# Performance work log

Measured on AMD Instinct MI355X. Metric: run time of the kernel, lower is better.

Reference implementation:

```python
import jax, jax.numpy as jnp
import numpy as np

NUM_EMBEDDINGS = 8192
EMBEDDING_DIM = 512
COMMITMENT_COST = 0.1


def setup_inputs() -> dict:
    key = jax.random.key(0)
    k_z, k_cb = jax.random.split(key)
    z = jax.random.normal(k_z, (16, 1024, EMBEDDING_DIM), dtype=jnp.float32)
    # nn.Embedding weight init: uniform(-1/num_embeddings, 1/num_embeddings)
    bound = 1.0 / NUM_EMBEDDINGS
    codebook = jax.random.uniform(
        k_cb, (NUM_EMBEDDINGS, EMBEDDING_DIM), dtype=jnp.float32,
        minval=-bound, maxval=bound)
    return {"z": z, "codebook": codebook}


def reference(z, codebook):
    # z: [B, T, D], codebook: [K, D]
    zf = z.reshape(-1, z.shape[-1])                      # [N, D]
    # squared euclidean distances: ||z||^2 + ||e||^2 - 2 z e^T  -> [N, K]
    distances = (jnp.sum(zf * zf, axis=1, keepdims=True)
                 + jnp.sum(codebook * codebook, axis=1)
                 - 2.0 * jnp.matmul(zf, codebook.T))
    indices = jnp.argmin(distances, axis=1)              # [N]
    z_quantized = codebook[indices].reshape(z.shape)     # [B, T, D]
    zq_sg = jax.lax.stop_gradient(z_quantized)
    commitment_loss = jnp.mean((zq_sg - z) ** 2)
    # mse(z, zq.detach()) == mse(zq.detach(), z) == commitment_loss
    vq_loss = commitment_loss + COMMITMENT_COST * commitment_loss
    # straight-through estimator
    z_st = z + jax.lax.stop_gradient(z_quantized - z)
    return (z_st, vq_loss)
```

## Files before the change

kernel.cpp:

```cpp
#include <hip/hip_runtime.h>


#define M_ROWS 16384
#define K_CODES 8192
#define DIM 512
#define BM 128
#define BN 128
#define BK 128
#define NT (K_CODES / BN)
#define OUT0_SIZE (M_ROWS * DIM)
#define GB_BLOCKS 1024

typedef int   i32x8 __attribute__((ext_vector_type(8)));
typedef float f32x4 __attribute__((ext_vector_type(4)));

template <bool HI>
__device__ __forceinline__ int pk8(float a, float b, int old) {
    return __builtin_amdgcn_cvt_pk_fp8_f32(a, b, old, HI);
}

__device__ __forceinline__ void gload_lds(const unsigned char* g, unsigned char* l) {
    __builtin_amdgcn_global_load_lds((const __attribute__((address_space(1))) void*)g,
                                     (__attribute__((address_space(3))) void*)l, 16, 0, 0);
}

__global__ __launch_bounds__(256) void convert_all(
    const float* __restrict__ z, const float* __restrict__ cb,
    unsigned char* __restrict__ z8, unsigned char* __restrict__ cb8,
    float* __restrict__ enorm, unsigned int* __restrict__ candMin,
    float* __restrict__ lossSlot)
{
    const int tid = threadIdx.x;
    if (blockIdx.x == 0 && tid == 0) *lossSlot = 0.f;
    {
        int gi = blockIdx.x * 256 + tid;
        if (gi < M_ROWS) candMin[gi] = 0xFFFFFFFFu;
    }
    if (blockIdx.x < K_CODES / 4) {
        const int w = tid >> 6, lane = tid & 63;
        const int row = blockIdx.x * 4 + w;
        const float* src = cb + (size_t)row * DIM + lane * 8;
        float4 a = *(const float4*)(src);
        float4 b = *(const float4*)(src + 4);
        float ns = a.x * a.x + a.y * a.y + a.z * a.z + a.w * a.w
                 + b.x * b.x + b.y * b.y + b.z * b.z + b.w * b.w;
        const float S = 8192.0f;
        int lo = 0, hi = 0;
        lo = pk8<false>(a.x * S, a.y * S, lo); lo = pk8<true>(a.z * S, a.w * S, lo);
        hi = pk8<false>(b.x * S, b.y * S, hi); hi = pk8<true>(b.z * S, b.w * S, hi);
        *(int2*)(cb8 + (size_t)row * DIM + lane * 8) = make_int2(lo, hi);
        for (int m = 32; m; m >>= 1) ns += __shfl_down(ns, m, 64);
        if (lane == 0) enorm[row] = S * ns;
    } else {
        size_t i = ((size_t)(blockIdx.x - K_CODES / 4) * 256 + tid) * 8;
        float4 a = *(const float4*)(z + i);
        float4 b = *(const float4*)(z + i + 4);
        int lo = 0, hi = 0;
        lo = pk8<false>(a.x, a.y, lo); lo = pk8<true>(a.z, a.w, lo);
        hi = pk8<false>(b.x, b.y, hi); hi = pk8<true>(b.z, b.w, hi);
        *(int2*)(z8 + i) = make_int2(lo, hi);
    }
}

__global__ __launch_bounds__(256, 2) void gemm_argmin(
    const unsigned char* __restrict__ z8, const unsigned char* __restrict__ cbb,
    const float* __restrict__ enorm, unsigned int* __restrict__ candMin)
{
    __shared__ alignas(32) unsigned char As[2 * BM * BK];
    __shared__ alignas(32) unsigned char Bs[2 * BN * BK];
    __shared__ float Es[BN];

    const int tid = threadIdx.x;
    const int lane = tid & 63;
    const int w = tid >> 6;
    const int b = blockIdx.x;
    const int xcd = b & 7;
    const int idx = b >> 3;
    const int ktile = idx >> 4;
    const int mtile = xcd * 16 + (idx & 15);
    const int mbase = mtile * BM;
    const int nbase = ktile * BN;

    if (tid < BN) Es[tid] = enorm[nbase + tid];

    f32x4 acc[16];
#pragma unroll
    for (int i = 0; i < 16; ++i) acc[i] = (f32x4){0.f, 0.f, 0.f, 0.f};

    const int rA = lane >> 3;
    const int jG = ((lane & 7) ^ rA) * 16;
    const int quad = lane >> 4;
    const int l15 = lane & 15;
    const int sw = l15 & 7;
    const int rw = (w >> 1) * 64;
    const int cw = (w & 1) * 64;
    const int t32 = ((quad << 1) ^ (sw & 6)) * 16;

#define STAGE(buf, dt_) do {                                                  \
    _Pragma("unroll")                                                         \
    for (int i_ = 0; i_ < 4; ++i_) {                                          \
        int c_ = w * 4 + i_;                                                  \
        int row_ = c_ * 8 + rA;                                               \
        int col_ = (dt_) * BK + jG;                                           \
        gload_lds(z8 + (size_t)(mbase + row_) * DIM + col_,                   \
                  As + (buf) * (BM * BK) + c_ * 1024 + lane * 16);            \
        gload_lds(cbb + (size_t)(nbase + row_) * DIM + col_,                  \
                  Bs + (buf) * (BN * BK) + c_ * 1024 + lane * 16);            \
    } } while (0)

    STAGE(0, 0);
    __syncthreads();

#pragma unroll 1
    for (int dt = 0; dt < 4; ++dt) {
        const int cur = dt & 1;
        if (dt < 3) STAGE(cur ^ 1, dt + 1);
        const unsigned char* Ab = As + cur * (BM * BK);
        const unsigned char* Bb = Bs + cur * (BN * BK);
#pragma unroll
        for (int h = 0; h < 2; ++h) {
            i32x8 bf0 = *(const i32x8*)(Bb + (cw + (h * 2 + 0) * 16 + l15) * BK + t32);
            i32x8 bf1 = *(const i32x8*)(Bb + (cw + (h * 2 + 1) * 16 + l15) * BK + t32);
#pragma unroll
            for (int rf = 0; rf < 4; ++rf) {
                i32x8 a = *(const i32x8*)(Ab + (rw + rf * 16 + l15) * BK + t32);
                acc[rf * 4 + h * 2 + 0] = __builtin_amdgcn_mfma_scale_f32_16x16x128_f8f6f4(
                    a, bf0, acc[rf * 4 + h * 2 + 0],
                    0, 0, 0, 0x7F7F7F7F, 0, 0x7F7F7F7F);
                acc[rf * 4 + h * 2 + 1] = __builtin_amdgcn_mfma_scale_f32_16x16x128_f8f6f4(
                    a, bf1, acc[rf * 4 + h * 2 + 1],
                    0, 0, 0, 0x7F7F7F7F, 0, 0x7F7F7F7F);
            }
        }
        __syncthreads();
    }
#undef STAGE

    float es[4];
#pragma unroll
    for (int cf = 0; cf < 4; ++cf) es[cf] = Es[cw + cf * 16 + l15];

#pragma unroll
    for (int rf = 0; rf < 4; ++rf) {
#pragma unroll
        for (int r = 0; r < 4; ++r) {
            float bv = 3.4e38f; int bi = 0;
#pragma unroll
            for (int cf = 0; cf < 4; ++cf) {
                int col = cw + cf * 16 + l15;
                float dist = fmaf(-2.0f, acc[rf * 4 + cf][r], es[cf]);
                if (dist < bv) { bv = dist; bi = col; }
            }
            unsigned u = __builtin_bit_cast(unsigned, bv);
            u ^= ((unsigned)(((int)u) >> 31)) | 0x80000000u;
            unsigned key = (u & 0xFFFFE000u) | (unsigned)(nbase + bi);
#pragma unroll
            for (int m = 1; m < 16; m <<= 1) {
                unsigned o = __shfl_xor(key, m, 64);
                key = o < key ? o : key;
            }
            if (l15 == 0)
                atomicMin(&candMin[mbase + rw + rf * 16 + quad * 4 + r], key);
        }
    }
}

__global__ __launch_bounds__(256) void gather_out(
    const float* __restrict__ z, const float* __restrict__ cb,
    const unsigned int* __restrict__ candMin, float* __restrict__ out)
{
    __shared__ float red[4];
    const int tid = threadIdx.x;
    const int w = tid >> 6, lane = tid & 63;
    float lsum = 0.f;
#pragma unroll
    for (int it = 0; it < M_ROWS / (GB_BLOCKS * 4); ++it) {
        int row = (it * GB_BLOCKS + blockIdx.x) * 4 + w;
        int k = (int)(candMin[row] & 8191u);
#pragma unroll
        for (int j = 0; j < 2; ++j) {
            int slot = lane + j * 64;
            float4 zv = ((const float4*)(z + (size_t)row * DIM))[slot];
            float4 cv = ((const float4*)(cb + (size_t)k * DIM))[slot];
            float dx = cv.x - zv.x, dy = cv.y - zv.y;
            float dz2 = cv.z - zv.z, dw = cv.w - zv.w;
            float4 o = {zv.x + dx, zv.y + dy, zv.z + dz2, zv.w + dw};
            ((float4*)(out + (size_t)row * DIM))[slot] = o;
            lsum += dx * dx + dy * dy + dz2 * dz2 + dw * dw;
        }
    }
    for (int m = 32; m; m >>= 1) lsum += __shfl_down(lsum, m, 64);
    if (lane == 0) red[w] = lsum;
    __syncthreads();
    if (tid == 0) {
        float t = (red[0] + red[1]) + (red[2] + red[3]);
        atomicAdd(out + OUT0_SIZE, t * (1.1f / (float)OUT0_SIZE));
    }
}

extern "C" void kernel_launch(void* const* d_in, const int* in_sizes, int n_in,
                              void* d_out, int out_size, void* d_ws, size_t ws_size,
                              hipStream_t stream) {
    const float* z = (const float*)d_in[0];
    const float* cb = (const float*)d_in[1];
    float* out = (float*)d_out;
    char* ws = (char*)d_ws;

    unsigned char* z8     = (unsigned char*)(ws);
    unsigned char* cb8    = (unsigned char*)(ws + 8388608);
    float* enorm          = (float*)(ws + 12582912);
    unsigned int* candMin = (unsigned int*)(ws + 12615680);

    convert_all<<<K_CODES / 4 + M_ROWS * DIM / 2048, 256, 0, stream>>>(
        z, cb, z8, cb8, enorm, candMin, out + OUT0_SIZE);
    gemm_argmin<<<NT * (M_ROWS / BM), 256, 0, stream>>>(z8, cb8, enorm, candMin);
    gather_out<<<GB_BLOCKS, 256, 0, stream>>>(z, cb, candMin, out);
}
```

Measured before the change: 249.3 us.

## Single-buffer GEMM LDS tiles to raise occupancy to four blocks per CU

Replaces the double-buffered LDS staging in the fp8 GEMM/argmin kernel with a single buffer (32KB instead of 64KB) and raises the launch-bounds minimum blocks per CU from 2 to 4. The aim is to hide global-load latency through more resident blocks rather than software prefetch. In exchange, each block now waits on its own loads every K-step and adds a barrier per iteration. Tighter register limits could also cause spills with the 16 accumulator vectors.

```diff
diff --git a/kernel.cpp b/kernel.cpp
--- a/kernel.cpp
+++ b/kernel.cpp
@@ -62,12 +62,12 @@
     }
 }
 
-__global__ __launch_bounds__(256, 2) void gemm_argmin(
+__global__ __launch_bounds__(256, 4) void gemm_argmin(
     const unsigned char* __restrict__ z8, const unsigned char* __restrict__ cbb,
     const float* __restrict__ enorm, unsigned int* __restrict__ candMin)
 {
-    __shared__ alignas(32) unsigned char As[2 * BM * BK];
-    __shared__ alignas(32) unsigned char Bs[2 * BN * BK];
+    __shared__ alignas(32) unsigned char As[BM * BK];
+    __shared__ alignas(32) unsigned char Bs[BN * BK];
     __shared__ float Es[BN];
 
     const int tid = threadIdx.x;
@@ -96,34 +96,26 @@
     const int cw = (w & 1) * 64;
     const int t32 = ((quad << 1) ^ (sw & 6)) * 16;
 
-#define STAGE(buf, dt_) do {                                                  \
-    _Pragma("unroll")                                                         \
-    for (int i_ = 0; i_ < 4; ++i_) {                                          \
-        int c_ = w * 4 + i_;                                                  \
-        int row_ = c_ * 8 + rA;                                               \
-        int col_ = (dt_) * BK + jG;                                           \
-        gload_lds(z8 + (size_t)(mbase + row_) * DIM + col_,                   \
-                  As + (buf) * (BM * BK) + c_ * 1024 + lane * 16);            \
-        gload_lds(cbb + (size_t)(nbase + row_) * DIM + col_,                  \
-                  Bs + (buf) * (BN * BK) + c_ * 1024 + lane * 16);            \
-    } } while (0)
-
-    STAGE(0, 0);
-    __syncthreads();
-
 #pragma unroll 1
     for (int dt = 0; dt < 4; ++dt) {
-        const int cur = dt & 1;
-        if (dt < 3) STAGE(cur ^ 1, dt + 1);
-        const unsigned char* Ab = As + cur * (BM * BK);
-        const unsigned char* Bb = Bs + cur * (BN * BK);
+#pragma unroll
+        for (int i_ = 0; i_ < 4; ++i_) {
+            int c_ = w * 4 + i_;
+            int row_ = c_ * 8 + rA;
+            int col_ = dt * BK + jG;
+            gload_lds(z8 + (size_t)(mbase + row_) * DIM + col_,
+                      As + c_ * 1024 + lane * 16);
+            gload_lds(cbb + (size_t)(nbase + row_) * DIM + col_,
+                      Bs + c_ * 1024 + lane * 16);
+        }
+        __syncthreads();
 #pragma unroll
         for (int h = 0; h < 2; ++h) {
-            i32x8 bf0 = *(const i32x8*)(Bb + (cw + (h * 2 + 0) * 16 + l15) * BK + t32);
-            i32x8 bf1 = *(const i32x8*)(Bb + (cw + (h * 2 + 1) * 16 + l15) * BK + t32);
+            i32x8 bf0 = *(const i32x8*)(Bs + (cw + (h * 2 + 0) * 16 + l15) * BK + t32);
+            i32x8 bf1 = *(const i32x8*)(Bs + (cw + (h * 2 + 1) * 16 + l15) * BK + t32);
 #pragma unroll
             for (int rf = 0; rf < 4; ++rf) {
-                i32x8 a = *(const i32x8*)(Ab + (rw + rf * 16 + l15) * BK + t32);
+                i32x8 a = *(const i32x8*)(As + (rw + rf * 16 + l15) * BK + t32);
                 acc[rf * 4 + h * 2 + 0] = __builtin_amdgcn_mfma_scale_f32_16x16x128_f8f6f4(
                     a, bf0, acc[rf * 4 + h * 2 + 0],
                     0, 0, 0, 0x7F7F7F7F, 0, 0x7F7F7F7F);
@@ -134,7 +126,6 @@
         }
         __syncthreads();
     }
-#undef STAGE
 
     float es[4];
 #pragma unroll
```

Result: slower. 261.5 us (+4.9%).
